# Performance work log

Measured on AMD Instinct MI355X. Metric: run time of the kernel, lower is better.

Reference implementation:

```python
import jax, jax.numpy as jnp
import numpy as np

D_MODEL = 1024
N_HEADS = 16
D_KEYS = 64
D_LLM = 1024
LN_EPS = 1e-12


def setup_inputs() -> dict:
    key = jax.random.key(0)
    ks = jax.random.split(key, 14)
    B, L, S = 2, 2048, 2048
    AH = N_HEADS * D_KEYS  # all_head_size = 1024
    w = 0.02
    return {
        "target_embedding": jax.random.normal(ks[0], (B, L, D_MODEL), jnp.float32),
        "source_embedding": jax.random.normal(ks[1], (S, D_LLM), jnp.float32),
        "value_embedding": jax.random.normal(ks[2], (S, D_LLM), jnp.float32),
        "Wq": jax.random.normal(ks[3], (D_MODEL, AH), jnp.float32) * w,
        "bq": jnp.zeros((AH,), jnp.float32),
        "Wk": jax.random.normal(ks[4], (D_LLM, AH), jnp.float32) * w,
        "bk": jnp.zeros((AH,), jnp.float32),
        "Wv": jax.random.normal(ks[5], (D_LLM, AH), jnp.float32) * w,
        "bv": jnp.zeros((AH,), jnp.float32),
        "Wo": jax.random.normal(ks[6], (AH, D_MODEL), jnp.float32) * w,
        "bo": jnp.zeros((D_MODEL,), jnp.float32),
        "ln_g": jnp.ones((D_MODEL,), jnp.float32),
        "ln_b": jnp.zeros((D_MODEL,), jnp.float32),
    }


def reference(target_embedding, source_embedding, value_embedding,
              Wq, bq, Wk, bk, Wv, bv, Wo, bo, ln_g, ln_b):
    B, L, _ = target_embedding.shape
    S = source_embedding.shape[0]
    H, E = N_HEADS, D_KEYS

    q = (target_embedding @ Wq + bq).reshape(B, L, H, E)
    k = (source_embedding @ Wk + bk).reshape(S, H, E)
    v = (value_embedding @ Wv + bv).reshape(S, H, E)

    eq = jax.nn.elu(q)
    ek = jax.nn.elu(k)
    qn = eq / jnp.linalg.norm(eq, axis=-1, keepdims=True)  # L2-normalize per head vector
    kn = ek / jnp.linalg.norm(ek, axis=-1, keepdims=True)

    scores = jnp.einsum('blhe,she->bhls', qn, kn)
    scale = 1.0 / np.sqrt(E).astype(np.float32)
    A = jax.nn.softmax(scale * scores, axis=-1)  # dropout is identity in eval

    ctx = jnp.einsum('bhls,she->blhe', A, v).reshape(B, L, H * E)
    h = ctx @ Wo + bo

    x = h + target_embedding
    mu = jnp.mean(x, axis=-1, keepdims=True)
    var = jnp.mean(jnp.square(x - mu), axis=-1, keepdims=True)
    return (x - mu) / jnp.sqrt(var + LN_EPS) * ln_g + ln_b
```

## Files before the change

### kernel.cpp

```cpp
#include <hip/hip_runtime.h>
#include <math.h>

typedef unsigned short u16t;
typedef __attribute__((ext_vector_type(8))) __bf16 bf16x8;
typedef __attribute__((ext_vector_type(4))) float f32x4;
typedef __attribute__((ext_vector_type(16))) float f32x16;
typedef __attribute__((ext_vector_type(4))) unsigned short u16x4;

__device__ __forceinline__ u16t f2bf(float f) {
  union { float f; unsigned u; } v; v.f = f;
  return (u16t)((v.u + 0x7FFFu + ((v.u >> 16) & 1u)) >> 16);
}
__device__ __forceinline__ float bf2f(u16t u) {
  union { unsigned u; float f; } v; v.u = (unsigned)u << 16; return v.f;
}

__device__ __forceinline__ void gload_lds16(const void* g, void* l) {
  __builtin_amdgcn_global_load_lds(
      (__attribute__((address_space(1))) void*)(uintptr_t)g,
      (__attribute__((address_space(3))) void*)(unsigned)(uintptr_t)l,
      16, 0, 0);
}

__device__ __forceinline__ f32x16 mf32(bf16x8 a, bf16x8 b, f32x16 c) {
  return __builtin_amdgcn_mfma_f32_32x32x16_bf16(a, b, c, 0, 0, 0);
}

__global__ __launch_bounds__(256) void k_cvt3(const float* __restrict__ t0,
                                              const float* __restrict__ s0,
                                              const float* __restrict__ v0,
                                              u16t* __restrict__ out) {
  int row = blockIdx.x, t = threadIdx.x;
  const float* src = row < 4096 ? t0 + ((size_t)row << 10)
                   : row < 6144 ? s0 + ((size_t)(row - 4096) << 10)
                                : v0 + ((size_t)(row - 6144) << 10);
  f32x4 x = *reinterpret_cast<const f32x4*>(src + t * 4);
  u16x4 y;
#pragma unroll
  for (int j = 0; j < 4; j++) y[j] = f2bf(x[j]);
  *reinterpret_cast<u16x4*>(out + ((size_t)row << 10) + t * 4) = y;
}

__global__ __launch_bounds__(256) void k_wtrans4(const float* __restrict__ Wq,
                                                 const float* __restrict__ Wk,
                                                 const float* __restrict__ Wv,
                                                 const float* __restrict__ Wo,
                                                 u16t* __restrict__ dstAll,
                                                 float* __restrict__ KVcol,
                                                 float* __restrict__ rsums) {
  __shared__ u16t tile[64][68];
  int z = blockIdx.z;
  const float* in = z == 0 ? Wq : z == 1 ? Wk : z == 2 ? Wv : Wo;
  u16t* out = dstAll + ((size_t)z << 20);
  int r0 = blockIdx.y * 64, c0 = blockIdx.x * 64;
  int t = threadIdx.x;
  if (z == 0 && blockIdx.y == 0) {
    int g = blockIdx.x * 256 + t;
    if (g < 2048) KVcol[g] = 0.f;
    rsums[g] = 0.f;
    rsums[g + 4096] = 0.f;
  }
  int rr = t >> 4, q4 = (t & 15) * 4;
#pragma unroll
  for (int i = 0; i < 4; i++) {
    int r = rr + i * 16;
    f32x4 x = *reinterpret_cast<const f32x4*>(&in[(size_t)(r0 + r) * 1024 + c0 + q4]);
#pragma unroll
    for (int j = 0; j < 4; j++) tile[r][q4 + j] = f2bf(x[j]);
  }
  __syncthreads();
#pragma unroll
  for (int i = 0; i < 4; i++) {
    int c = rr + i * 16;
    u16x4 y;
#pragma unroll
    for (int j = 0; j < 4; j++) y[j] = tile[q4 + j][c];
    *reinterpret_cast<u16x4*>(&out[(size_t)(c0 + c) * 1024 + r0 + q4]) = y;
  }
}

__global__ __launch_bounds__(256) void k_vtrans2(const u16t* __restrict__ in0,
                                                 const u16t* __restrict__ in1,
                                                 u16t* __restrict__ o0,
                                                 u16t* __restrict__ o1) {
  __shared__ u16t tile[64][68];
  int z = blockIdx.z;
  const u16t* in = z ? in1 : in0;
  u16t* out = z ? o1 : o0;
  int r0 = blockIdx.y * 64, c0 = blockIdx.x * 64;
  int t = threadIdx.x;
  int rr = t >> 4, q4 = (t & 15) * 4;
#pragma unroll
  for (int i = 0; i < 4; i++) {
    int r = rr + i * 16;
    u16x4 x = *reinterpret_cast<const u16x4*>(&in[(size_t)(r0 + r) * 1024 + c0 + q4]);
#pragma unroll
    for (int j = 0; j < 4; j++) tile[r][q4 + j] = x[j];
  }
  __syncthreads();
#pragma unroll
  for (int i = 0; i < 4; i++) {
    int c = rr + i * 16;
    u16x4 y;
#pragma unroll
    for (int j = 0; j < 4; j++) y[j] = tile[q4 + j][c];
    *reinterpret_cast<u16x4*>(&out[(size_t)(c0 + c) * 2048 + r0 + q4]) = y;
  }
}

__global__ __launch_bounds__(256) void k_colsum2(const u16t* __restrict__ kn,
                                                 const u16t* __restrict__ vb,
                                                 float* __restrict__ Kcol,
                                                 float* __restrict__ Vcol) {
  int t = threadIdx.x, c4 = t * 4, r0 = blockIdx.x * 32;
  float sk[4] = {0.f, 0.f, 0.f, 0.f}, sv[4] = {0.f, 0.f, 0.f, 0.f};
  for (int r = r0; r < r0 + 32; r++) {
    u16x4 a = *reinterpret_cast<const u16x4*>(&kn[((size_t)r << 10) + c4]);
    u16x4 b = *reinterpret_cast<const u16x4*>(&vb[((size_t)r << 10) + c4]);
#pragma unroll
    for (int j = 0; j < 4; j++) { sk[j] += bf2f(a[j]); sv[j] += bf2f(b[j]); }
  }
#pragma unroll
  for (int j = 0; j < 4; j++) {
    atomicAdd(&Kcol[c4 + j], sk[j]);
    atomicAdd(&Vcol[c4 + j], sv[j]);
  }
}

__global__ __launch_bounds__(256) void k_ktv(const u16t* __restrict__ knT,
                                             const u16t* __restrict__ vT,
                                             const float* __restrict__ Kcol,
                                             u16t* __restrict__ MT) {
  __shared__ float sls[4][1024];
  int qd = blockIdx.x, h = blockIdx.y;
  int e1t = qd >> 1, e2t = qd & 1;
  int t = threadIdx.x, lane = t & 63, w = t >> 6;
  int l31 = lane & 31, hi = lane >> 5;
  const u16t* ap = knT + (((size_t)((h << 6) + e1t * 32 + l31)) << 11) + w * 512 + hi * 8;
  const u16t* bp = vT  + (((size_t)((h << 6) + e2t * 32 + l31)) << 11) + w * 512 + hi * 8;
  f32x16 acc = {};
#pragma unroll
  for (int k = 0; k < 32; k++) {
    bf16x8 a = *(const bf16x8*)(ap + k * 16);
    bf16x8 b = *(const bf16x8*)(bp + k * 16);
    acc = mf32(a, b, acc);
  }
#pragma unroll
  for (int r = 0; r < 16; r++) {
    int e1l = (r & 3) + 8 * (r >> 2) + 4 * hi;
    sls[w][e1l * 32 + l31] = acc[r];
  }
  __syncthreads();
#pragma unroll
  for (int i = 0; i < 4; i++) {
    int idx = t * 4 + i;
    int e1 = idx >> 5, e2 = idx & 31;
    float s = sls[0][idx] + sls[1][idx] + sls[2][idx] + sls[3][idx];
    MT[h * 4160 + (e2t * 32 + e2) * 64 + e1t * 32 + e1] = f2bf(s);
  }
  if (qd == 0 && t < 64)
    MT[h * 4160 + 4096 + t] = f2bf(Kcol[(h << 6) + t]);
}

__global__ __launch_bounds__(256) void k_ctx(const u16t* __restrict__ qn8,
                                             const u16t* __restrict__ MT,
                                             const float* __restrict__ Vcol,
                                             u16t* __restrict__ ctx) {
  int rt = blockIdx.x;
  int t = threadIdx.x, lane = t & 63, w = t >> 6;
  int l31 = lane & 31, hi = lane >> 5;
  int rowb = rt * 32;
  const u16t* qbase = qn8 + (((size_t)(rowb + l31)) << 10) + hi * 8;
  const f32x16 fz = {};
#pragma unroll
  for (int hh = 0; hh < 4; hh++) {
    int h = w * 4 + hh;
    const u16t* mbase = MT + h * 4160;
    bf16x8 af[4], kf[4];
#pragma unroll
    for (int ks = 0; ks < 4; ks++) {
      af[ks] = *(const bf16x8*)(qbase + (h << 6) + ks * 16);
      kf[ks] = *(const bf16x8*)(mbase + 4096 + ks * 16 + hi * 8);
    }
    f32x16 a0, a1, rd;
#pragma unroll
    for (int ks = 0; ks < 4; ks++) {
      bf16x8 b0 = *(const bf16x8*)(mbase + l31 * 64 + ks * 16 + hi * 8);
      bf16x8 b1 = *(const bf16x8*)(mbase + (32 + l31) * 64 + ks * 16 + hi * 8);
      a0 = mf32(af[ks], b0, ks ? a0 : fz);
      a1 = mf32(af[ks], b1, ks ? a1 : fz);
      rd = mf32(af[ks], kf[ks], ks ? rd : fz);
    }
    float vc0 = Vcol[(h << 6) + l31];
    float vc1 = Vcol[(h << 6) + 32 + l31];
#pragma unroll
    for (int r = 0; r < 16; r++) {
      int row = rowb + (r & 3) + 8 * (r >> 2) + 4 * hi;
      float ri = 1.f / (2048.f + rd[r]);
      u16t* cp = ctx + (((size_t)row) << 10) + (h << 6) + l31;
      cp[0]  = f2bf((a0[r] + vc0) * ri);
      cp[32] = f2bf((a1[r] + vc1) * ri);
    }
  }
}

__device__ __forceinline__ void gemm128_acc8(const u16t* __restrict__ A,
                                             const u16t* __restrict__ Bt,
                                             int m0, int n0, f32x4 acc[2][4]) {
  __shared__ __align__(16) u16t As[2][128 * 64];
  __shared__ __align__(16) u16t Bs[2][128 * 64];
  int t = threadIdx.x, lane = t & 63, w = t >> 6;
  int l15 = lane & 15, l16 = lane >> 4;
  int wr = w >> 1, wc = w & 1;
  int srow = t >> 3;
  int slc = ((t & 7) ^ (srow & 7)) << 3;

#define GSTAGE(KT, NB) do {                                                      \
    _Pragma("unroll")                                                            \
    for (int i = 0; i < 2; i++) {                                                \
      int row_ = srow + i * 64;                                                  \
      int c16_ = (t + i * 512) * 16;                                             \
      gload_lds16(A + ((size_t)(m0 + row_) << 10) + (KT) + slc, (char*)As[NB] + c16_); \
      gload_lds16(Bt + ((size_t)(n0 + row_) << 10) + (KT) + slc, (char*)Bs[NB] + c16_); \
    } } while (0)

  GSTAGE(0, 0);
  for (int ki = 0; ki < 16; ki++) {
    int cur = ki & 1;
    if (ki < 15) {
      GSTAGE((ki + 1) << 6, cur ^ 1);
      asm volatile("s_waitcnt vmcnt(4)" ::: "memory");
    } else {
      asm volatile("s_waitcnt vmcnt(0)" ::: "memory");
    }
    __builtin_amdgcn_s_barrier();
    asm volatile("" ::: "memory");
#pragma unroll
    for (int kk = 0; kk < 2; kk++) {
      bf16x8 af[2], bfr[4];
#pragma unroll
      for (int m = 0; m < 2; m++) {
        int ar = wr * 32 + m * 16 + l15;
        af[m] = *(const bf16x8*)((char*)As[cur] + ar * 128 + ((kk * 64 + l16 * 16) ^ ((ar & 7) << 4)));
      }
#pragma unroll
      for (int n = 0; n < 4; n++) {
        int br = wc * 64 + n * 16 + l15;
        bfr[n] = *(const bf16x8*)((char*)Bs[cur] + br * 128 + ((kk * 64 + l16 * 16) ^ ((br & 7) << 4)));
      }
#pragma unroll
      for (int m = 0; m < 2; m++)
#pragma unroll
        for (int n = 0; n < 4; n++)
          acc[m][n] = __builtin_amdgcn_mfma_f32_16x16x32_bf16(af[m], bfr[n], acc[m][n], 0, 0, 0);
    }
    __builtin_amdgcn_s_barrier();
    asm volatile("" ::: "memory");
  }
#undef GSTAGE
}

__global__ __launch_bounds__(512) void k_gemm_qkv(const u16t* __restrict__ A,
                                                  const u16t* __restrict__ Wt,
                                                  const float* __restrict__ b0,
                                                  const float* __restrict__ b1,
                                                  const float* __restrict__ b2,
                                                  u16t* __restrict__ out) {
  int bid = blockIdx.y * 8 + blockIdx.x;
  int swz = (bid & 7) * 64 + (bid >> 3);
  int n0 = (swz & 7) * 128, m0 = (swz >> 3) * 128;
  int seg = (m0 >= 6144) ? 2 : (m0 >= 4096) ? 1 : 0;
  const float* bias = (seg == 0) ? b0 : (seg == 1) ? b1 : b2;
  f32x4 acc[2][4] = {};
  gemm128_acc8(A, Wt + ((size_t)seg << 20), m0, n0, acc);

  int t = threadIdx.x, lane = t & 63, w = t >> 6;
  int l15 = lane & 15, l16 = lane >> 4;
  int wr = w >> 1, wc = w & 1;
  float bb[4];
#pragma unroll
  for (int n = 0; n < 4; n++) bb[n] = bias[n0 + wc * 64 + n * 16 + l15];
  if (seg < 2) {
    float scale0 = (seg == 0) ? 0.125f : 1.f;
#pragma unroll
    for (int m = 0; m < 2; m++) {
#pragma unroll
      for (int r = 0; r < 4; r++) {
        float e[4]; float ss = 0.f;
#pragma unroll
        for (int n = 0; n < 4; n++) {
          float x = acc[m][n][r] + bb[n];
          e[n] = x > 0.f ? x : (__expf(x) - 1.f);
          ss += e[n] * e[n];
        }
        ss += __shfl_xor(ss, 1); ss += __shfl_xor(ss, 2);
        ss += __shfl_xor(ss, 4); ss += __shfl_xor(ss, 8);
        float rinv = rsqrtf(ss) * scale0;
        int row = m0 + wr * 32 + m * 16 + l16 * 4 + r;
#pragma unroll
        for (int n = 0; n < 4; n++)
          out[((size_t)row << 10) + n0 + wc * 64 + n * 16 + l15] = f2bf(e[n] * rinv);
      }
    }
  } else {
#pragma unroll
    for (int m = 0; m < 2; m++) {
      int row = m0 + wr * 32 + m * 16 + l16 * 4;
#pragma unroll
      for (int n = 0; n < 4; n++) {
        int col = n0 + wc * 64 + n * 16 + l15;
#pragma unroll
        for (int r = 0; r < 4; r++)
          out[((size_t)(row + r) << 10) + col] = f2bf(acc[m][n][r] + bb[n]);
      }
    }
  }
}

__global__ __launch_bounds__(512) void k_gemm_o(const u16t* __restrict__ A,
                                                const u16t* __restrict__ Wt,
                                                const float* __restrict__ bias,
                                                const float* __restrict__ target,
                                                u16t* __restrict__ Hb,
                                                float* __restrict__ rsums) {
  int bid = blockIdx.y * 8 + blockIdx.x;
  int swz = (bid & 7) * 32 + (bid >> 3);
  int n0 = (swz & 7) * 128, m0 = (swz >> 3) * 128;
  f32x4 acc[2][4] = {};
  gemm128_acc8(A, Wt, m0, n0, acc);
  int t = threadIdx.x, lane = t & 63, w = t >> 6;
  int l15 = lane & 15, l16 = lane >> 4;
  int wr = w >> 1, wc = w & 1;
  float bb[4];
#pragma unroll
  for (int n = 0; n < 4; n++) bb[n] = bias[n0 + wc * 64 + n * 16 + l15];
#pragma unroll
  for (int m = 0; m < 2; m++) {
#pragma unroll
    for (int r = 0; r < 4; r++) {
      int row = m0 + wr * 32 + m * 16 + l16 * 4 + r;
      float s = 0.f, ss = 0.f;
      float xs[4];
#pragma unroll
      for (int n = 0; n < 4; n++) {
        int col = n0 + wc * 64 + n * 16 + l15;
        float x = acc[m][n][r] + bb[n] + target[((size_t)row << 10) + col];
        xs[n] = x; s += x; ss = fmaf(x, x, ss);
      }
#pragma unroll
      for (int n = 0; n < 4; n++)
        Hb[((size_t)row << 10) + n0 + wc * 64 + n * 16 + l15] = f2bf(xs[n]);
      s += __shfl_xor(s, 1); ss += __shfl_xor(ss, 1);
      s += __shfl_xor(s, 2); ss += __shfl_xor(ss, 2);
      s += __shfl_xor(s, 4); ss += __shfl_xor(ss, 4);
      s += __shfl_xor(s, 8); ss += __shfl_xor(ss, 8);
      if (l15 == 0) {
        atomicAdd(&rsums[row * 2], s);
        atomicAdd(&rsums[row * 2 + 1], ss);
      }
    }
  }
}

__global__ __launch_bounds__(256) void k_out_ln(const u16t* __restrict__ Hb,
                                                const float* __restrict__ rsums,
                                                const float* __restrict__ g,
                                                const float* __restrict__ bb,
                                                float* __restrict__ out) {
  int row = blockIdx.x, t = threadIdx.x;
  u16x4 hx = *reinterpret_cast<const u16x4*>(Hb + ((size_t)row << 10) + t * 4);
  float s = rsums[row * 2], ss = rsums[row * 2 + 1];
  float mu = s * (1.f / 1024.f);
  float var = ss * (1.f / 1024.f) - mu * mu;
  float rsn = rsqrtf(var + 1e-12f);
  f32x4 gv = *reinterpret_cast<const f32x4*>(&g[t * 4]);
  f32x4 bv = *reinterpret_cast<const f32x4*>(&bb[t * 4]);
  f32x4 o;
#pragma unroll
  for (int j = 0; j < 4; j++) o[j] = (bf2f(hx[j]) - mu) * rsn * gv[j] + bv[j];
  *reinterpret_cast<f32x4*>(&out[(size_t)row * 1024 + t * 4]) = o;
}

extern "C" void kernel_launch(void* const* d_in, const int* in_sizes, int n_in,
                              void* d_out, int out_size, void* d_ws, size_t ws_size,
                              hipStream_t stream) {
  const float* target = (const float*)d_in[0];
  const float* source = (const float*)d_in[1];
  const float* value  = (const float*)d_in[2];
  const float* Wq = (const float*)d_in[3];
  const float* bq = (const float*)d_in[4];
  const float* Wk = (const float*)d_in[5];
  const float* bk = (const float*)d_in[6];
  const float* Wv = (const float*)d_in[7];
  const float* bvp = (const float*)d_in[8];
  const float* Wo = (const float*)d_in[9];
  const float* bo = (const float*)d_in[10];
  const float* lng = (const float*)d_in[11];
  const float* lnb = (const float*)d_in[12];
  float* out = (float*)d_out;
  char* ws = (char*)d_ws;
  const size_t MB = 1u << 20;

  u16t* abf   = (u16t*)ws;
  u16t* ctxb  = (u16t*)ws;
  u16t* Wt    = (u16t*)(ws + 16 * MB);
  u16t* Wot   = Wt + ((size_t)3 << 20);
  u16t* qkvnb = (u16t*)(ws + 24 * MB);
  u16t* qnb   = qkvnb;
  u16t* knb   = qkvnb + ((size_t)4096 << 10);
  u16t* vbf   = qkvnb + ((size_t)6144 << 10);
  u16t* knT   = (u16t*)(ws + 40 * MB);
  u16t* vTb   = (u16t*)(ws + 44 * MB);
  u16t* Hb    = (u16t*)(ws + 48 * MB);
  float* Kcolf = (float*)(ws + 64 * MB);
  float* Vcolf = Kcolf + 1024;
  u16t* MTb   = (u16t*)(Vcolf + 1024);
  float* rsums = (float*)(ws + 65 * MB);

  k_cvt3<<<dim3(8192), 256, 0, stream>>>(target, source, value, abf);
  k_wtrans4<<<dim3(16, 16, 4), 256, 0, stream>>>(Wq, Wk, Wv, Wo, Wt, Kcolf, rsums);
  k_gemm_qkv<<<dim3(8, 64), 512, 0, stream>>>(abf, Wt, bq, bk, bvp, qkvnb);
  k_colsum2<<<dim3(64), 256, 0, stream>>>(knb, vbf, Kcolf, Vcolf);
  k_vtrans2<<<dim3(16, 32, 2), 256, 0, stream>>>(knb, vbf, knT, vTb);
  k_ktv<<<dim3(4, 16), 256, 0, stream>>>(knT, vTb, Kcolf, MTb);
  k_ctx<<<dim3(128), 256, 0, stream>>>(qnb, MTb, Vcolf, ctxb);
  k_gemm_o<<<dim3(8, 32), 512, 0, stream>>>(ctxb, Wot, bo, target, Hb, rsums);
  k_out_ln<<<dim3(4096), 256, 0, stream>>>(Hb, rsums, lng, lnb, out);
}
```

Before: 99.15 us.

## Fuse K/V transpose and column sums into QKV GEMM epilogue

The QKV GEMM epilogue now writes normalized K and V directly in transposed layout and accumulates per-column sums with wave shuffles plus atomics, removing the separate colsum and transpose kernels. This eliminates two launches and a full round-trip of K/V through global memory. The transposed stores write 4 bf16 per lane at a 4KB stride, which may be less coalesced than the previous row stores.

```diff
diff --git a/kernel.cpp b/kernel.cpp
--- a/kernel.cpp
+++ b/kernel.cpp
@@ -79,54 +79,6 @@
   }
 }
 
-__global__ __launch_bounds__(256) void k_vtrans2(const u16t* __restrict__ in0,
-                                                 const u16t* __restrict__ in1,
-                                                 u16t* __restrict__ o0,
-                                                 u16t* __restrict__ o1) {
-  __shared__ u16t tile[64][68];
-  int z = blockIdx.z;
-  const u16t* in = z ? in1 : in0;
-  u16t* out = z ? o1 : o0;
-  int r0 = blockIdx.y * 64, c0 = blockIdx.x * 64;
-  int t = threadIdx.x;
-  int rr = t >> 4, q4 = (t & 15) * 4;
-#pragma unroll
-  for (int i = 0; i < 4; i++) {
-    int r = rr + i * 16;
-    u16x4 x = *reinterpret_cast<const u16x4*>(&in[(size_t)(r0 + r) * 1024 + c0 + q4]);
-#pragma unroll
-    for (int j = 0; j < 4; j++) tile[r][q4 + j] = x[j];
-  }
-  __syncthreads();
-#pragma unroll
-  for (int i = 0; i < 4; i++) {
-    int c = rr + i * 16;
-    u16x4 y;
-#pragma unroll
-    for (int j = 0; j < 4; j++) y[j] = tile[q4 + j][c];
-    *reinterpret_cast<u16x4*>(&out[(size_t)(c0 + c) * 2048 + r0 + q4]) = y;
-  }
-}
-
-__global__ __launch_bounds__(256) void k_colsum2(const u16t* __restrict__ kn,
-                                                 const u16t* __restrict__ vb,
-                                                 float* __restrict__ Kcol,
-                                                 float* __restrict__ Vcol) {
-  int t = threadIdx.x, c4 = t * 4, r0 = blockIdx.x * 32;
-  float sk[4] = {0.f, 0.f, 0.f, 0.f}, sv[4] = {0.f, 0.f, 0.f, 0.f};
-  for (int r = r0; r < r0 + 32; r++) {
-    u16x4 a = *reinterpret_cast<const u16x4*>(&kn[((size_t)r << 10) + c4]);
-    u16x4 b = *reinterpret_cast<const u16x4*>(&vb[((size_t)r << 10) + c4]);
-#pragma unroll
-    for (int j = 0; j < 4; j++) { sk[j] += bf2f(a[j]); sv[j] += bf2f(b[j]); }
-  }
-#pragma unroll
-  for (int j = 0; j < 4; j++) {
-    atomicAdd(&Kcol[c4 + j], sk[j]);
-    atomicAdd(&Vcol[c4 + j], sv[j]);
-  }
-}
-
 __global__ __launch_bounds__(256) void k_ktv(const u16t* __restrict__ knT,
                                              const u16t* __restrict__ vT,
                                              const float* __restrict__ Kcol,
@@ -265,7 +217,11 @@
                                                   const float* __restrict__ b0,
                                                   const float* __restrict__ b1,
                                                   const float* __restrict__ b2,
-                                                  u16t* __restrict__ out) {
+                                                  u16t* __restrict__ qn8,
+                                                  u16t* __restrict__ knT,
+                                                  u16t* __restrict__ vT,
+                                                  float* __restrict__ Kcol,
+                                                  float* __restrict__ Vcol) {
   int bid = blockIdx.y * 8 + blockIdx.x;
   int swz = (bid & 7) * 64 + (bid >> 3);
   int n0 = (swz & 7) * 128, m0 = (swz >> 3) * 128;
@@ -280,8 +236,8 @@
   float bb[4];
 #pragma unroll
   for (int n = 0; n < 4; n++) bb[n] = bias[n0 + wc * 64 + n * 16 + l15];
-  if (seg < 2) {
-    float scale0 = (seg == 0) ? 0.125f : 1.f;
+
+  if (seg == 0) {
 #pragma unroll
     for (int m = 0; m < 2; m++) {
 #pragma unroll
@@ -295,24 +251,56 @@
         }
         ss += __shfl_xor(ss, 1); ss += __shfl_xor(ss, 2);
         ss += __shfl_xor(ss, 4); ss += __shfl_xor(ss, 8);
-        float rinv = rsqrtf(ss) * scale0;
+        float rinv = rsqrtf(ss) * 0.125f;
         int row = m0 + wr * 32 + m * 16 + l16 * 4 + r;
 #pragma unroll
         for (int n = 0; n < 4; n++)
-          out[((size_t)row << 10) + n0 + wc * 64 + n * 16 + l15] = f2bf(e[n] * rinv);
+          qn8[((size_t)row << 10) + n0 + wc * 64 + n * 16 + l15] = f2bf(e[n] * rinv);
       }
     }
   } else {
+    u16t* outT = (seg == 1) ? knT : vT;
+    float* colp = (seg == 1) ? Kcol : Vcol;
+    int mloc = m0 - ((seg == 1) ? 4096 : 6144);
+    float cs[4] = {0.f, 0.f, 0.f, 0.f};
 #pragma unroll
     for (int m = 0; m < 2; m++) {
-      int row = m0 + wr * 32 + m * 16 + l16 * 4;
+      u16x4 tv[4];
+#pragma unroll
+      for (int r = 0; r < 4; r++) {
+        float v[4];
+        if (seg == 1) {
+          float e[4]; float ss = 0.f;
+#pragma unroll
+          for (int n = 0; n < 4; n++) {
+            float x = acc[m][n][r] + bb[n];
+            e[n] = x > 0.f ? x : (__expf(x) - 1.f);
+            ss += e[n] * e[n];
+          }
+          ss += __shfl_xor(ss, 1); ss += __shfl_xor(ss, 2);
+          ss += __shfl_xor(ss, 4); ss += __shfl_xor(ss, 8);
+          float rinv = rsqrtf(ss);
+#pragma unroll
+          for (int n = 0; n < 4; n++) v[n] = e[n] * rinv;
+        } else {
+#pragma unroll
+          for (int n = 0; n < 4; n++) v[n] = acc[m][n][r] + bb[n];
+        }
+#pragma unroll
+        for (int n = 0; n < 4; n++) { tv[n][r] = f2bf(v[n]); cs[n] += v[n]; }
+      }
+      int rowb = mloc + wr * 32 + m * 16 + l16 * 4;
 #pragma unroll
       for (int n = 0; n < 4; n++) {
         int col = n0 + wc * 64 + n * 16 + l15;
-#pragma unroll
-        for (int r = 0; r < 4; r++)
-          out[((size_t)(row + r) << 10) + col] = f2bf(acc[m][n][r] + bb[n]);
-      }
+        *reinterpret_cast<u16x4*>(outT + ((size_t)col << 11) + rowb) = tv[n];
+      }
+    }
+#pragma unroll
+    for (int n = 0; n < 4; n++) {
+      float s = cs[n];
+      s += __shfl_xor(s, 16); s += __shfl_xor(s, 32);
+      if (l16 == 0) atomicAdd(&colp[n0 + wc * 64 + n * 16 + l15], s);
     }
   }
 }
@@ -405,10 +393,7 @@
   u16t* ctxb  = (u16t*)ws;
   u16t* Wt    = (u16t*)(ws + 16 * MB);
   u16t* Wot   = Wt + ((size_t)3 << 20);
-  u16t* qkvnb = (u16t*)(ws + 24 * MB);
-  u16t* qnb   = qkvnb;
-  u16t* knb   = qkvnb + ((size_t)4096 << 10);
-  u16t* vbf   = qkvnb + ((size_t)6144 << 10);
+  u16t* qnb   = (u16t*)(ws + 24 * MB);
   u16t* knT   = (u16t*)(ws + 40 * MB);
   u16t* vTb   = (u16t*)(ws + 44 * MB);
   u16t* Hb    = (u16t*)(ws + 48 * MB);
@@ -419,9 +404,7 @@
 
   k_cvt3<<<dim3(8192), 256, 0, stream>>>(target, source, value, abf);
   k_wtrans4<<<dim3(16, 16, 4), 256, 0, stream>>>(Wq, Wk, Wv, Wo, Wt, Kcolf, rsums);
-  k_gemm_qkv<<<dim3(8, 64), 512, 0, stream>>>(abf, Wt, bq, bk, bvp, qkvnb);
-  k_colsum2<<<dim3(64), 256, 0, stream>>>(knb, vbf, Kcolf, Vcolf);
-  k_vtrans2<<<dim3(16, 32, 2), 256, 0, stream>>>(knb, vbf, knT, vTb);
+  k_gemm_qkv<<<dim3(8, 64), 512, 0, stream>>>(abf, Wt, bq, bk, bvp, qnb, knT, vTb, Kcolf, Vcolf);
   k_ktv<<<dim3(4, 16), 256, 0, stream>>>(knT, vTb, Kcolf, MTb);
   k_ctx<<<dim3(128), 256, 0, stream>>>(qnb, MTb, Vcolf, ctxb);
   k_gemm_o<<<dim3(8, 32), 512, 0, stream>>>(ctxb, Wot, bo, target, Hb, rsums);
```

Measured after the change: 87.19 us. 1.14x faster.
